# Kernel tuning notes

Hardware: AMD Instinct MI355X
Metric: run time of the kernel (lower is better)

The kernel has to match this reference:

```python
import jax, jax.numpy as jnp
import numpy as np

N = 8192      # nodes
E = 131072    # edges (avg degree 16)
MUL = 128     # multiplicity of 0e and 1o channels
A = 10        # node_attrs (element one-hot) dim
RB = 8        # radial basis size
INV_SQRT3 = 0.5773502691896258  # w3j normalization for l=1 paths


def _lin0(x, W):
    # e3nn-style Linear on scalar (l=0) channels, 1/sqrt(fan_in) normalization
    return (x @ W) / jnp.sqrt(jnp.asarray(W.shape[0], x.dtype))


def _lin1(v, W):
    # e3nn-style Linear on l=1 channels: mixes multiplicities, acts identically on the 3 components
    return jnp.einsum('nuc,uw->nwc', v, W) / jnp.sqrt(jnp.asarray(W.shape[0], v.dtype))


def setup_inputs() -> dict:
    key = jax.random.key(0)
    ks = jax.random.split(key, 26)
    f32 = jnp.float32
    w = lambda k, s: jax.random.normal(k, s, f32)
    D_EF = RB + 2 * MUL  # 264: radial basis + source + target scalar embeddings
    return {
        'node_attrs': jax.random.uniform(ks[0], (N, A), f32),
        'node_feats': w(ks[1], (N, 4 * MUL)),
        'edge_attrs': w(ks[2], (E, 4)),
        'edge_feats': jax.random.uniform(ks[3], (E, RB), f32),
        'edge_index': jax.random.randint(ks[4], (2, E), 0, N, jnp.int32),
        'W_skip_s': w(ks[5], (MUL, MUL)), 'W_skip_v': w(ks[6], (MUL, MUL)),
        'W_up_s': w(ks[7], (MUL, MUL)), 'W_up_v': w(ks[8], (MUL, MUL)),
        'W_src': w(ks[9], (A, MUL)), 'W_tgt': w(ks[10], (A, MUL)),
        'W_r0': w(ks[11], (D_EF, 64)), 'W_r1': w(ks[12], (64, 64)),
        'W_r2': w(ks[13], (64, 64)), 'W_r3': w(ks[14], (64, 4 * MUL)),
        'W_d0': w(ks[15], (D_EF, 64)), 'W_d1': w(ks[16], (64, 1)),
        'W1_s': w(ks[17], (2 * MUL, 2 * MUL)), 'W1_v': w(ks[18], (2 * MUL, MUL)),
        'Wres_s': w(ks[19], (MUL, 2 * MUL)), 'Wres_v': w(ks[20], (MUL, MUL)),
        'W2_s': w(ks[21], (MUL, MUL)), 'W2_v': w(ks[22], (MUL, MUL)),
        'alpha': jnp.asarray(20.0, f32), 'beta': jnp.asarray(0.0, f32),
    }


def reference(node_attrs, node_feats, edge_attrs, edge_feats, edge_index,
              W_skip_s, W_skip_v, W_up_s, W_up_v, W_src, W_tgt,
              W_r0, W_r1, W_r2, W_r3, W_d0, W_d1,
              W1_s, W1_v, Wres_s, Wres_v, W2_s, W2_v, alpha, beta):
    n = node_feats.shape[0]
    s = node_feats[:, :MUL]                       # [N,128] 0e
    v = node_feats[:, MUL:].reshape(n, MUL, 3)    # [N,128,3] 1o
    # skip_tp: Linear(node_feats -> hidden)
    sc = jnp.concatenate([_lin0(s, W_skip_s), _lin1(v, W_skip_v).reshape(n, -1)], axis=-1)
    # linear_up: Linear(node_feats -> edge_irreps)
    us, uv = _lin0(s, W_up_s), _lin1(v, W_up_v)
    # source/target scalar embeddings from node_attrs
    src_e = _lin0(node_attrs, W_src)
    tgt_e = _lin0(node_attrs, W_tgt)
    snd, rcv = edge_index[0], edge_index[1]
    ef = jnp.concatenate([edge_feats, src_e[snd], tgt_e[rcv]], axis=-1)   # [E,264]
    # radial MLP -> per-edge tensor product weights
    h = jax.nn.silu(_lin0(ef, W_r0))
    h = jax.nn.silu(_lin0(h, W_r1))
    h = jax.nn.silu(_lin0(h, W_r2))
    tpw = _lin0(h, W_r3)                          # [E, 4*128]
    # edge density -> per-node density via scatter-sum
    d = jax.nn.silu(_lin0(ef, W_d0))
    edge_density = jnp.tanh(_lin0(d, W_d1) ** 2)  # [E,1]
    density = jax.ops.segment_sum(edge_density, rcv, num_segments=n)      # [N,1]
    # sparse CG tensor product (uvu), paths: 0x0->0e, 0x1->1o, 1x0->1o, 1x1->0e
    xs, xv = us[snd], uv[snd]                     # gather sender features
    y0, y1 = edge_attrs[:, 0], edge_attrs[:, 1:4]
    w1, w2, w3, w4 = jnp.split(tpw, 4, axis=-1)
    m0a = w1 * xs * y0[:, None]                                          # 0e x 0e -> 0e
    m0b = w4 * jnp.einsum('euc,ec->eu', xv, y1) * INV_SQRT3              # 1o x 1o -> 0e
    m1a = (w2 * xs)[:, :, None] * y1[:, None, :] * INV_SQRT3             # 0e x 1o -> 1o
    m1b = w3[:, :, None] * xv * y0[:, None, None] * INV_SQRT3            # 1o x 0e -> 1o
    mid_s = jnp.concatenate([m0a, m0b], axis=1)   # [E,256] irreps_mid scalars
    mid_v = jnp.concatenate([m1a, m1b], axis=1)   # [E,256,3] irreps_mid vectors
    msg_s = jax.ops.segment_sum(mid_s, rcv, num_segments=n)
    msg_v = jax.ops.segment_sum(mid_v, rcv, num_segments=n)
    # linear_1 + learned density normalization
    denom = density * beta + alpha                # [N,1]
    m_s = _lin0(msg_s, W1_s) / denom
    m_v = _lin1(msg_v, W1_v) / denom[..., None]
    # linear_res on up-projected node feats
    m_s = m_s + _lin0(us, Wres_s)                 # [N,256]: 128 scalars + 128 gates
    m_v = m_v + _lin1(uv, Wres_v)                 # [N,128,3]
    # Gate: silu on scalars, sigmoid gates on vectors
    out_s = jax.nn.silu(m_s[:, :MUL])
    out_v = m_v * jax.nn.sigmoid(m_s[:, MUL:])[:, :, None]
    # linear_2
    f_s = _lin0(out_s, W2_s)
    f_v = _lin1(out_v, W2_v)
    # reshape_irreps -> [N, mul, 1+3]
    out = jnp.concatenate([f_s[:, :, None], f_v], axis=2)
    return out, sc
```

## Files before the change

kernel.cpp:

```cpp
#include <hip/hip_runtime.h>

#define NN 8192
#define EE 131072
#define MUL 128
#define AA 10
#define RB 8
#define DEF 264
#define INV_SQRT3 0.5773502691896258f
#define INV_SQRT128 0.08838834764831845f
#define INV_SQRT10 0.31622776601683794f
#define INV_SQRT264 0.06154574548966636f

typedef __attribute__((ext_vector_type(8))) short short8;
typedef __attribute__((ext_vector_type(4))) float floatx4;

#define WS_XQ     ((size_t)0)
#define WS_USB    (WS_XQ    + (size_t)NN*256)
#define WS_UVB    (WS_USB   + (size_t)NN*64)
#define WS_SRC    (WS_UVB   + (size_t)NN*192)
#define WS_TGT    (WS_SRC   + (size_t)NN*64)
#define WS_MSGSB  (WS_TGT   + (size_t)NN*64)
#define WS_MSGVB  (WS_MSGSB + (size_t)NN*128)
#define WS_GATE   (WS_MSGVB + (size_t)NN*384)
#define WS_COUNTS (WS_GATE  + (size_t)NN*128)
#define WS_OFFS   (WS_COUNTS+ (size_t)NN)
#define WS_CURSOR (WS_OFFS  + (size_t)(NN+4))
#define WS_POS    (WS_CURSOR+ (size_t)NN)
#define WS_META   (WS_POS   + (size_t)EE)
#define WS_TPW    (WS_META  + (size_t)EE*8)
#define WS_WB     (WS_TPW   + (size_t)EE*256)
#define WS_WP     (WS_WB    + (size_t)152*256)
#define WS_WN     (WS_WP    + (size_t)352*256)

__device__ __forceinline__ float silu_f(float x) {
    return x * __builtin_amdgcn_rcpf(1.f + __expf(-x));
}
__device__ __forceinline__ float sigm_f(float x) {
    return __builtin_amdgcn_rcpf(1.f + __expf(-x));
}

__device__ __forceinline__ unsigned short f2bf(float x) {
    union { float f; unsigned u; } uf; uf.f = x;
    unsigned r = uf.u + 0x7FFFu + ((uf.u >> 16) & 1u);
    return (unsigned short)(r >> 16);
}

__global__ __launch_bounds__(256) void csr_count(
    const int* __restrict__ edge_index, int* __restrict__ counts)
{
    int e = blockIdx.x * 256 + threadIdx.x;
    atomicAdd(&counts[edge_index[EE + e]], 1);
}

__global__ __launch_bounds__(1024) void csr_scan(
    const int* __restrict__ counts, int* __restrict__ offs, int* __restrict__ cursor)
{
    __shared__ int sums[1024];
    const int t = threadIdx.x;
    int local[8];
    int s = 0;
#pragma unroll
    for (int k = 0; k < 8; ++k) { local[k] = s; s += counts[t * 8 + k]; }
    sums[t] = s;
    __syncthreads();
    for (int d = 1; d < 1024; d <<= 1) {
        int v = (t >= d) ? sums[t - d] : 0;
        __syncthreads();
        sums[t] += v;
        __syncthreads();
    }
    int base = (t > 0) ? sums[t - 1] : 0;
#pragma unroll
    for (int k = 0; k < 8; ++k) {
        offs[t * 8 + k] = base + local[k];
        cursor[t * 8 + k] = base + local[k];
    }
    if (t == 1023) offs[8192] = sums[1023];
}

__global__ __launch_bounds__(256) void csr_scatter(
    const int* __restrict__ edge_index, int* __restrict__ cursor, int* __restrict__ pos)
{
    int e = blockIdx.x * 256 + threadIdx.x;
    pos[e] = atomicAdd(&cursor[edge_index[EE + e]], 1);
}

__global__ __launch_bounds__(256) void swizzle_weights(
    const float* __restrict__ Wr0, const float* __restrict__ Wd0,
    const float* __restrict__ Wr1, const float* __restrict__ Wr2,
    const float* __restrict__ Wr3, unsigned short* __restrict__ WBall)
{
    int fid = blockIdx.x * 256 + threadIdx.x;
    int lane = fid & 63;
    int frag = fid >> 6;
    int k0 = (lane >> 4) * 8;
    int n0 = lane & 15;
    unsigned short o[8];

    if (frag < 72) {
        int kt = frag >> 3, nt = frag & 7;
        int n = nt * 16 + n0;
#pragma unroll
        for (int j = 0; j < 8; ++j) {
            int k = kt * 32 + k0 + j;
            float v = 0.f;
            if (k < 264) v = ((n < 64) ? Wr0[k * 64 + n] : Wd0[k * 64 + (n - 64)]) * INV_SQRT264;
            o[j] = f2bf(v);
        }
    } else if (frag < 80) {
        int fl = frag - 72;
        int kt = fl >> 2, nt = fl & 3;
        int n = nt * 16 + n0;
#pragma unroll
        for (int j = 0; j < 8; ++j)
            o[j] = f2bf(Wr1[(kt * 32 + k0 + j) * 64 + n] * 0.125f);
    } else if (frag < 88) {
        int fl = frag - 80;
        int kt = fl >> 2, nt = fl & 3;
        int n = nt * 16 + n0;
#pragma unroll
        for (int j = 0; j < 8; ++j)
            o[j] = f2bf(Wr2[(kt * 32 + k0 + j) * 64 + n] * 0.125f);
    } else {
        int fl = frag - 88;
        int kt = fl >> 5, nt = fl & 31;
        int n = nt * 16 + n0;
        int q = n >> 6;
        float sc = (q < 2) ? 0.125f : 0.125f * INV_SQRT3;
#pragma unroll
        for (int j = 0; j < 8; ++j)
            o[j] = f2bf(Wr3[(kt * 32 + k0 + j) * 512 + n] * sc);
    }
    uint4 pk;
    pk.x = (unsigned)o[0] | ((unsigned)o[1] << 16);
    pk.y = (unsigned)o[2] | ((unsigned)o[3] << 16);
    pk.z = (unsigned)o[4] | ((unsigned)o[5] << 16);
    pk.w = (unsigned)o[6] | ((unsigned)o[7] << 16);
    *(uint4*)(WBall + (size_t)fid * 8) = pk;
}

__global__ __launch_bounds__(256) void swizzle_post(
    const float* __restrict__ W1s, const float* __restrict__ W1v,
    const float* __restrict__ Wrs, const float* __restrict__ Wrv,
    const float* __restrict__ W2s, const float* __restrict__ W2v,
    unsigned short* __restrict__ WPall)
{
    int fid = blockIdx.x * 256 + threadIdx.x;
    int lane = fid & 63;
    int frag = fid >> 6;
    int k0 = (lane >> 4) * 8;
    int n0 = lane & 15;
    unsigned short o[8];

    if (frag < 192) {
        int kt = frag >> 4, nt = frag & 15;
        int n = nt * 16 + n0;
#pragma unroll
        for (int j = 0; j < 8; ++j) {
            int k = kt * 32 + k0 + j;
            float v = (k < 256) ? W1s[k * 256 + n] * 0.0625f
                                : Wrs[(k - 256) * 256 + n] * INV_SQRT128;
            o[j] = f2bf(v);
        }
    } else if (frag < 288) {
        int fl = frag - 192;
        int kt = fl >> 3, nt = fl & 7;
        int n = nt * 16 + n0;
#pragma unroll
        for (int j = 0; j < 8; ++j) {
            int k = kt * 32 + k0 + j;
            float v = (k < 256) ? W1v[k * 128 + n] * 0.0625f
                                : Wrv[(k - 256) * 128 + n] * INV_SQRT128;
            o[j] = f2bf(v);
        }
    } else if (frag < 320) {
        int fl = frag - 288;
        int kt = fl >> 3, nt = fl & 7;
        int n = nt * 16 + n0;
#pragma unroll
        for (int j = 0; j < 8; ++j)
            o[j] = f2bf(W2s[(kt * 32 + k0 + j) * 128 + n] * INV_SQRT128);
    } else {
        int fl = frag - 320;
        int kt = fl >> 3, nt = fl & 7;
        int n = nt * 16 + n0;
#pragma unroll
        for (int j = 0; j < 8; ++j)
            o[j] = f2bf(W2v[(kt * 32 + k0 + j) * 128 + n] * INV_SQRT128);
    }
    uint4 pk;
    pk.x = (unsigned)o[0] | ((unsigned)o[1] << 16);
    pk.y = (unsigned)o[2] | ((unsigned)o[3] << 16);
    pk.z = (unsigned)o[4] | ((unsigned)o[5] << 16);
    pk.w = (unsigned)o[6] | ((unsigned)o[7] << 16);
    *(uint4*)(WPall + (size_t)fid * 8) = pk;
}

__global__ __launch_bounds__(256) void swizzle_node(
    const float* __restrict__ Wss, const float* __restrict__ Wus,
    const float* __restrict__ Wsv, const float* __restrict__ Wuv,
    const float* __restrict__ Wsrc, const float* __restrict__ Wtgt,
    unsigned short* __restrict__ WN)
{
    int fid = blockIdx.x * 256 + threadIdx.x;
    int lane = fid & 63;
    int frag = fid >> 6;
    int k0 = (lane >> 4) * 8;
    int m0 = lane & 15;
    unsigned short o[8];

    if (frag < 128) {
        int g = frag >> 5;
        int fl = frag & 31;
        int kt = fl >> 3, mt = fl & 7;
        const float* W = (g == 0) ? Wss : (g == 1) ? Wus : (g == 2) ? Wsv : Wuv;
        int m = mt * 16 + m0;
#pragma unroll
        for (int j = 0; j < 8; ++j)
            o[j] = f2bf(W[(kt * 32 + k0 + j) * 128 + m] * INV_SQRT128);
    } else {
        int g = (frag - 128) >> 3;
        int mt = frag & 7;
        const float* W = g ? Wtgt : Wsrc;
        int m = mt * 16 + m0;
#pragma unroll
        for (int j = 0; j < 8; ++j) {
            int k = k0 + j;
            o[j] = f2bf((k < AA) ? W[k * 128 + m] * INV_SQRT10 : 0.f);
        }
    }
    uint4 pk;
    pk.x = (unsigned)o[0] | ((unsigned)o[1] << 16);
    pk.y = (unsigned)o[2] | ((unsigned)o[3] << 16);
    pk.z = (unsigned)o[4] | ((unsigned)o[5] << 16);
    pk.w = (unsigned)o[6] | ((unsigned)o[7] << 16);
    *(uint4*)(WN + (size_t)fid * 8) = pk;
}

#define PNB 16
__global__ __launch_bounds__(256) void node_pre_mfma(
    const float* __restrict__ node_attrs, const float* __restrict__ node_feats,
    const unsigned short* __restrict__ WN,
    float* __restrict__ sc_out, uint2* __restrict__ xq,
    unsigned short* __restrict__ us_b, unsigned short* __restrict__ uv_b,
    unsigned short* __restrict__ srcEb, unsigned short* __restrict__ tgtEb)
{
    __shared__ __align__(16) unsigned short Xs[PNB][136];
    __shared__ __align__(16) unsigned short Xv[3][PNB][136];
    __shared__ __align__(16) unsigned short Xa[PNB][40];
    const int t = threadIdx.x;
    const int l = t & 63, w = t >> 6;
    const int quad = l >> 4, lr = l & 15;
    const int n0 = blockIdx.x * PNB;

    {
        const int r = t >> 4, m = t & 15;
        const float* src = node_feats + (size_t)(n0 + r) * 512;
        float4 s0 = *(const float4*)(src + 8 * m);
        float4 s1 = *(const float4*)(src + 8 * m + 4);
        uint4 sp;
        sp.x = (unsigned)f2bf(s0.x) | ((unsigned)f2bf(s0.y) << 16);
        sp.y = (unsigned)f2bf(s0.z) | ((unsigned)f2bf(s0.w) << 16);
        sp.z = (unsigned)f2bf(s1.x) | ((unsigned)f2bf(s1.y) << 16);
        sp.w = (unsigned)f2bf(s1.z) | ((unsigned)f2bf(s1.w) << 16);
        *(uint4*)&Xs[r][8 * m] = sp;

        float4 q[6];
#pragma unroll
        for (int jj = 0; jj < 6; ++jj)
            q[jj] = *(const float4*)(src + 128 + 24 * m + 4 * jj);
        const float* qf = &q[0].x;
        unsigned short vb[3][8];
#pragma unroll
        for (int u = 0; u < 8; ++u) {
#pragma unroll
            for (int c = 0; c < 3; ++c)
                vb[c][u] = f2bf(qf[u * 3 + c]);
        }
#pragma unroll
        for (int c = 0; c < 3; ++c) {
            uint4 vp;
            vp.x = (unsigned)vb[c][0] | ((unsigned)vb[c][1] << 16);
            vp.y = (unsigned)vb[c][2] | ((unsigned)vb[c][3] << 16);
            vp.z = (unsigned)vb[c][4] | ((unsigned)vb[c][5] << 16);
            vp.w = (unsigned)vb[c][6] | ((unsigned)vb[c][7] << 16);
            *(uint4*)&Xv[c][r][8 * m] = vp;
        }
    }
    for (int idx = t; idx < PNB * 32; idx += 256) {
        int r = idx >> 5, k = idx & 31;
        float v = (k < AA) ? node_attrs[(size_t)(n0 + r) * AA + k] : 0.f;
        Xa[r][k] = f2bf(v);
    }
    __syncthreads();

    const short8* WNf = (const short8*)WN;
    const int n = n0 + lr;

#pragma unroll
    for (int mi = 0; mi < 2; ++mi) {
        const int mt = w * 2 + mi;
        const int j0 = mt * 16 + quad * 4;

        floatx4 cSrc = (floatx4){0.f, 0.f, 0.f, 0.f};
        floatx4 cTgt = (floatx4){0.f, 0.f, 0.f, 0.f};
        {
            short8 ba = *(const short8*)&Xa[lr][quad * 8];
            cSrc = __builtin_amdgcn_mfma_f32_16x16x32_bf16(WNf[(size_t)(128 + mt) * 64 + l], ba, cSrc, 0, 0, 0);
            cTgt = __builtin_amdgcn_mfma_f32_16x16x32_bf16(WNf[(size_t)(136 + mt) * 64 + l], ba, cTgt, 0, 0, 0);
        }
        floatx4 cS = (floatx4){0.f, 0.f, 0.f, 0.f};
        floatx4 cU = (floatx4){0.f, 0.f, 0.f, 0.f};
#pragma unroll
        for (int kt = 0; kt < 4; ++kt) {
            short8 bs = *(const short8*)&Xs[lr][kt * 32 + quad * 8];
            cS = __builtin_amdgcn_mfma_f32_16x16x32_bf16(WNf[(size_t)(kt * 8 + mt) * 64 + l], bs, cS, 0, 0, 0);
            cU = __builtin_amdgcn_mfma_f32_16x16x32_bf16(WNf[(size_t)(32 + kt * 8 + mt) * 64 + l], bs, cU, 0, 0, 0);
        }
        floatx4 cSV[3], cUV[3];
#pragma unroll
        for (int c = 0; c < 3; ++c) {
            cSV[c] = (floatx4){0.f, 0.f, 0.f, 0.f};
            cUV[c] = (floatx4){0.f, 0.f, 0.f, 0.f};
#pragma unroll
            for (int kt = 0; kt < 4; ++kt) {
                short8 bv = *(const short8*)&Xv[c][lr][kt * 32 + quad * 8];
                cSV[c] = __builtin_amdgcn_mfma_f32_16x16x32_bf16(WNf[(size_t)(64 + kt * 8 + mt) * 64 + l], bv, cSV[c], 0, 0, 0);
                cUV[c] = __builtin_amdgcn_mfma_f32_16x16x32_bf16(WNf[(size_t)(96 + kt * 8 + mt) * 64 + l], bv, cUV[c], 0, 0, 0);
            }
        }

        {
            float4 o;
            o.x = cS[0]; o.y = cS[1]; o.z = cS[2]; o.w = cS[3];
            *(float4*)(sc_out + (size_t)n * 512 + j0) = o;
        }
        {
            float vv[12];
#pragma unroll
            for (int reg = 0; reg < 4; ++reg)
#pragma unroll
                for (int c = 0; c < 3; ++c) vv[reg * 3 + c] = cSV[c][reg];
            float* dst = sc_out + (size_t)n * 512 + 128 + j0 * 3;
#pragma unroll
            for (int qq = 0; qq < 3; ++qq) {
                float4 o;
                o.x = vv[qq * 4]; o.y = vv[qq * 4 + 1]; o.z = vv[qq * 4 + 2]; o.w = vv[qq * 4 + 3];
                *(float4*)(dst + qq * 4) = o;
            }
        }
        unsigned short ub[4], vxb[4], vyb[4], vzb[4];
#pragma unroll
        for (int reg = 0; reg < 4; ++reg) {
            ub[reg] = f2bf(cU[reg]);
            vxb[reg] = f2bf(cUV[0][reg]);
            vyb[reg] = f2bf(cUV[1][reg]);
            vzb[reg] = f2bf(cUV[2][reg]);
        }
        {
            uint2 p;
            p.x = (unsigned)ub[0] | ((unsigned)ub[1] << 16);
            p.y = (unsigned)ub[2] | ((unsigned)ub[3] << 16);
            *(uint2*)(us_b + (size_t)n * 128 + j0) = p;
        }
        {
            uint2 p;
            p.x = (unsigned)vxb[0] | ((unsigned)vxb[1] << 16);
            p.y = (unsigned)vxb[2] | ((unsigned)vxb[3] << 16);
            *(uint2*)(uv_b + ((size_t)0 * NN + n) * 128 + j0) = p;
            p.x = (unsigned)vyb[0] | ((unsigned)vyb[1] << 16);
            p.y = (unsigned)vyb[2] | ((unsigned)vyb[3] << 16);
            *(uint2*)(uv_b + ((size_t)1 * NN + n) * 128 + j0) = p;
            p.x = (unsigned)vzb[0] | ((unsigned)vzb[1] << 16);
            p.y = (unsigned)vzb[2] | ((unsigned)vzb[3] << 16);
            *(uint2*)(uv_b + ((size_t)2 * NN + n) * 128 + j0) = p;
        }
        {
            uint4 x0, x1;
            x0.x = (unsigned)ub[0] | ((unsigned)vxb[0] << 16);
            x0.y = (unsigned)vyb[0] | ((unsigned)vzb[0] << 16);
            x0.z = (unsigned)ub[1] | ((unsigned)vxb[1] << 16);
            x0.w = (unsigned)vyb[1] | ((unsigned)vzb[1] << 16);
            x1.x = (unsigned)ub[2] | ((unsigned)vxb[2] << 16);
            x1.y = (unsigned)vyb[2] | ((unsigned)vzb[2] << 16);
            x1.z = (unsigned)ub[3] | ((unsigned)vxb[3] << 16);
            x1.w = (unsigned)vyb[3] | ((unsigned)vzb[3] << 16);
            uint4* xp = (uint4*)(xq + (size_t)n * 128 + j0);
            xp[0] = x0; xp[1] = x1;
        }
        {
            uint2 p;
            p.x = (unsigned)f2bf(cSrc[0]) | ((unsigned)f2bf(cSrc[1]) << 16);
            p.y = (unsigned)f2bf(cSrc[2]) | ((unsigned)f2bf(cSrc[3]) << 16);
            *(uint2*)(srcEb + (size_t)n * 128 + j0) = p;
            p.x = (unsigned)f2bf(cTgt[0]) | ((unsigned)f2bf(cTgt[1]) << 16);
            p.y = (unsigned)f2bf(cTgt[2]) | ((unsigned)f2bf(cTgt[3]) << 16);
            *(uint2*)(tgtEb + (size_t)n * 128 + j0) = p;
        }
    }
}

#define EBK 64
#define H1OFF 80
#define HLD 152
__global__ __launch_bounds__(256, 4) void edge_mlp(
    const float* __restrict__ edge_attrs, const float* __restrict__ edge_feats,
    const int* __restrict__ edge_index,
    const unsigned short* __restrict__ srcEb, const unsigned short* __restrict__ tgtEb,
    const unsigned short* __restrict__ WB0, const unsigned short* __restrict__ WB1,
    const unsigned short* __restrict__ WB2, const unsigned short* __restrict__ WB3,
    const float* __restrict__ Wd1, const int* __restrict__ pos,
    unsigned short* __restrict__ tpwP, float* __restrict__ metaP)
{
    __shared__ __align__(16) unsigned short Hb[4][16][HLD];

    const int t = threadIdx.x;
    const int l = t & 63;
    const int w = t >> 6;
    const int quad = l >> 4;
    const int lr = l & 15;
    const int e0 = blockIdx.x * EBK + w * 16;

    const int eA = e0 + lr;
    const int sndA = edge_index[eA];
    const int rcvA = edge_index[EE + eA];
    const unsigned short* spp = srcEb + (size_t)sndA * 128;
    const unsigned short* tpp = tgtEb + (size_t)rcvA * 128;

    if (quad == 0) {
        float4 ya = *(const float4*)(edge_attrs + (size_t)eA * 4);
        float4 m;
        m.x = __int_as_float(sndA); m.y = ya.y; m.z = ya.z; m.w = ya.w;
        *(float4*)(metaP + (size_t)pos[eA] * 8) = m;
    }

    short8 afr[9];
    {
        const int cq = quad * 8;
        if (quad == 0) {
            float4 f0 = *(const float4*)(edge_feats + (size_t)eA * 8);
            float4 f1 = *(const float4*)(edge_feats + (size_t)eA * 8 + 4);
            union { short8 v; unsigned u[4]; } pk;
            pk.u[0] = (unsigned)f2bf(f0.x) | ((unsigned)f2bf(f0.y) << 16);
            pk.u[1] = (unsigned)f2bf(f0.z) | ((unsigned)f2bf(f0.w) << 16);
            pk.u[2] = (unsigned)f2bf(f1.x) | ((unsigned)f2bf(f1.y) << 16);
            pk.u[3] = (unsigned)f2bf(f1.z) | ((unsigned)f2bf(f1.w) << 16);
            afr[0] = pk.v;
        } else {
            afr[0] = *(const short8*)(spp + (cq - 8));
        }
#pragma unroll
        for (int kt = 1; kt < 9; ++kt) {
            const int c = kt * 32 + cq;
            if (c < 136) {
                afr[kt] = *(const short8*)(spp + (c - 8));
            } else if (c < 264) {
                afr[kt] = *(const short8*)(tpp + (c - 136));
            } else {
                short8 z = {0, 0, 0, 0, 0, 0, 0, 0};
                afr[kt] = z;
            }
        }
    }

    unsigned short (*H)[HLD] = Hb[w];

    {
        floatx4 c0[8];
#pragma unroll
        for (int nt = 0; nt < 8; ++nt) c0[nt] = (floatx4){0.f, 0.f, 0.f, 0.f};
#pragma unroll
        for (int kt = 0; kt < 9; ++kt) {
            const short8* bp = (const short8*)WB0 + (size_t)(kt * 8) * 64 + l;
#pragma unroll
            for (int nt = 0; nt < 8; ++nt)
                c0[nt] = __builtin_amdgcn_mfma_f32_16x16x32_bf16(afr[kt], bp[nt * 64], c0[nt], 0, 0, 0);
        }

#pragma unroll
        for (int nt = 0; nt < 4; ++nt)
#pragma unroll
            for (int reg = 0; reg < 4; ++reg)
                H[quad * 4 + reg][nt * 16 + lr] = f2bf(silu_f(c0[nt][reg]));

        float wd1v[4];
#pragma unroll
        for (int q2 = 0; q2 < 4; ++q2) wd1v[q2] = Wd1[q2 * 16 + lr] * 0.125f;
        float dp[4] = {0.f, 0.f, 0.f, 0.f};
#pragma unroll
        for (int nt = 0; nt < 4; ++nt)
#pragma unroll
            for (int reg = 0; reg < 4; ++reg)
                dp[reg] += silu_f(c0[nt + 4][reg]) * wd1v[nt];
#pragma unroll
        for (int m2 = 1; m2 < 16; m2 <<= 1) {
#pragma unroll
            for (int reg = 0; reg < 4; ++reg) dp[reg] += __shfl_xor(dp[reg], m2);
        }
        if (lr == 0) {
#pragma unroll
            for (int reg = 0; reg < 4; ++reg)
                metaP[(size_t)pos[e0 + quad * 4 + reg] * 8 + 4] = tanhf(dp[reg] * dp[reg]);
        }
    }

    const unsigned short* hrow0 = &H[lr][quad * 8];
    const unsigned short* hrow1 = &H[lr][H1OFF + quad * 8];

    {
        floatx4 c1[4];
#pragma unroll
        for (int nt = 0; nt < 4; ++nt) c1[nt] = (floatx4){0.f, 0.f, 0.f, 0.f};
#pragma unroll
        for (int kt = 0; kt < 2; ++kt) {
            short8 af = *(const short8*)(hrow0 + kt * 32);
            const short8* bp = (const short8*)WB1 + (size_t)(kt * 4) * 64 + l;
#pragma unroll
            for (int nt = 0; nt < 4; ++nt)
                c1[nt] = __builtin_amdgcn_mfma_f32_16x16x32_bf16(af, bp[nt * 64], c1[nt], 0, 0, 0);
        }
#pragma unroll
        for (int nt = 0; nt < 4; ++nt)
#pragma unroll
            for (int reg = 0; reg < 4; ++reg)
                H[quad * 4 + reg][H1OFF + nt * 16 + lr] = f2bf(silu_f(c1[nt][reg]));
    }

    {
        floatx4 c2[4];
#pragma unroll
        for (int nt = 0; nt < 4; ++nt) c2[nt] = (floatx4){0.f, 0.f, 0.f, 0.f};
#pragma unroll
        for (int kt = 0; kt < 2; ++kt) {
            short8 af = *(const short8*)(hrow1 + kt * 32);
            const short8* bp = (const short8*)WB2 + (size_t)(kt * 4) * 64 + l;
#pragma unroll
            for (int nt = 0; nt < 4; ++nt)
                c2[nt] = __builtin_amdgcn_mfma_f32_16x16x32_bf16(af, bp[nt * 64], c2[nt], 0, 0, 0);
        }
#pragma unroll
        for (int nt = 0; nt < 4; ++nt)
#pragma unroll
            for (int reg = 0; reg < 4; ++reg)
                H[quad * 4 + reg][nt * 16 + lr] = f2bf(silu_f(c2[nt][reg]));
    }

    {
        int slotr[4];
        float y0r[4];
#pragma unroll
        for (int reg = 0; reg < 4; ++reg) {
            const int er = e0 + quad * 4 + reg;
            slotr[reg] = pos[er];
            y0r[reg] = edge_attrs[(size_t)er * 4];
        }
        short8 af0 = *(const short8*)(hrow0);
        short8 af1 = *(const short8*)(hrow0 + 32);
        uint2* tpw2 = (uint2*)tpwP;
#pragma unroll
        for (int j2 = 0; j2 < 8; ++j2) {
            floatx4 c3[4];
#pragma unroll
            for (int g = 0; g < 4; ++g) c3[g] = (floatx4){0.f, 0.f, 0.f, 0.f};
#pragma unroll
            for (int g = 0; g < 4; ++g) {
                const short8* b0 = (const short8*)WB3 + (size_t)(g * 8 + j2) * 64 + l;
                const short8* b1 = (const short8*)WB3 + (size_t)(32 + g * 8 + j2) * 64 + l;
                c3[g] = __builtin_amdgcn_mfma_f32_16x16x32_bf16(af0, *b0, c3[g], 0, 0, 0);
                c3[g] = __builtin_amdgcn_mfma_f32_16x16x32_bf16(af1, *b1, c3[g], 0, 0, 0);
            }
            const int u = j2 * 16 + lr;
#pragma unroll
            for (int reg = 0; reg < 4; ++reg) {
                float w1v = c3[0][reg] * y0r[reg];
                float w2v = c3[1][reg];
                float w3v = c3[2][reg] * y0r[reg];
                float w4v = c3[3][reg];
                uint2 p;
                p.x = (unsigned)f2bf(w1v) | ((unsigned)f2bf(w2v) << 16);
                p.y = (unsigned)f2bf(w3v) | ((unsigned)f2bf(w4v) << 16);
                tpw2[(size_t)slotr[reg] * 128 + u] = p;
            }
        }
    }
}

__global__ __launch_bounds__(128) void node_gather(
    const unsigned short* __restrict__ tpwP, const float* __restrict__ metaP,
    const int* __restrict__ offs, const uint2* __restrict__ xq,
    const float* __restrict__ alpha_p, const float* __restrict__ beta_p,
    unsigned short* __restrict__ msgs_b, unsigned short* __restrict__ msgv_b)
{
    const int n = blockIdx.x;
    const int j = threadIdx.x;
    const int s0 = offs[n], s1 = offs[n + 1];
    const uint2* tpw2 = (const uint2*)tpwP;

    float as0 = 0.f, as1 = 0.f;
    float av0x = 0.f, av0y = 0.f, av0z = 0.f;
    float av1x = 0.f, av1y = 0.f, av1z = 0.f;
    float dsum = 0.f;

    int s = s0;
    for (; s + 4 <= s1; s += 4) {
        float4 ma[4]; float dn[4]; uint2 wv[4]; uint2 xv[4];
#pragma unroll
        for (int k = 0; k < 4; ++k) {
            ma[k] = *(const float4*)&metaP[(size_t)(s + k) * 8];
            dn[k] = metaP[(size_t)(s + k) * 8 + 4];
            wv[k] = tpw2[(size_t)(s + k) * 128 + j];
        }
#pragma unroll
        for (int k = 0; k < 4; ++k)
            xv[k] = xq[(size_t)__float_as_int(ma[k].x) * 128 + j];
#pragma unroll
        for (int k = 0; k < 4; ++k) {
            const float y1x = ma[k].y, y1y = ma[k].z, y1z = ma[k].w;
            dsum += dn[k];
            const float w1  = __uint_as_float(wv[k].x << 16);
            const float w2  = __uint_as_float(wv[k].x & 0xffff0000u);
            const float w3  = __uint_as_float(wv[k].y << 16);
            const float w4  = __uint_as_float(wv[k].y & 0xffff0000u);
            const float xs  = __uint_as_float(xv[k].x << 16);
            const float xvx = __uint_as_float(xv[k].x & 0xffff0000u);
            const float xvy = __uint_as_float(xv[k].y << 16);
            const float xvz = __uint_as_float(xv[k].y & 0xffff0000u);
            as0 += w1 * xs;
            as1 += w4 * (xvx * y1x + xvy * y1y + xvz * y1z);
            const float b2 = w2 * xs;
            av0x += b2 * y1x; av0y += b2 * y1y; av0z += b2 * y1z;
            av1x += w3 * xvx; av1y += w3 * xvy; av1z += w3 * xvz;
        }
    }
    for (; s < s1; ++s) {
        const float4 m0 = *(const float4*)&metaP[(size_t)s * 8];
        const float dns = metaP[(size_t)s * 8 + 4];
        const int snd = __float_as_int(m0.x);
        const float y1x = m0.y, y1y = m0.z, y1z = m0.w;
        dsum += dns;
        uint2 wv = tpw2[(size_t)s * 128 + j];
        uint2 xv = xq[(size_t)snd * 128 + j];
        const float w1  = __uint_as_float(wv.x << 16);
        const float w2  = __uint_as_float(wv.x & 0xffff0000u);
        const float w3  = __uint_as_float(wv.y << 16);
        const float w4  = __uint_as_float(wv.y & 0xffff0000u);
        const float xs  = __uint_as_float(xv.x << 16);
        const float xvx = __uint_as_float(xv.x & 0xffff0000u);
        const float xvy = __uint_as_float(xv.y << 16);
        const float xvz = __uint_as_float(xv.y & 0xffff0000u);
        as0 += w1 * xs;
        as1 += w4 * (xvx * y1x + xvy * y1y + xvz * y1z);
        const float b2 = w2 * xs;
        av0x += b2 * y1x; av0y += b2 * y1y; av0z += b2 * y1z;
        av1x += w3 * xvx; av1y += w3 * xvy; av1z += w3 * xvz;
    }

    const float invden = 1.f / (dsum * (*beta_p) + (*alpha_p));

    msgs_b[(size_t)n * 256 + j]       = f2bf(as0 * invden);
    msgs_b[(size_t)n * 256 + 128 + j] = f2bf(as1 * invden);
    msgv_b[((size_t)0 * NN + n) * 256 + j]       = f2bf(av0x * invden);
    msgv_b[((size_t)0 * NN + n) * 256 + 128 + j] = f2bf(av1x * invden);
    msgv_b[((size_t)1 * NN + n) * 256 + j]       = f2bf(av0y * invden);
    msgv_b[((size_t)1 * NN + n) * 256 + 128 + j] = f2bf(av1y * invden);
    msgv_b[((size_t)2 * NN + n) * 256 + j]       = f2bf(av0z * invden);
    msgv_b[((size_t)2 * NN + n) * 256 + 128 + j] = f2bf(av1z * invden);
}

#define DNP 16
__global__ __launch_bounds__(256) void post_fused(
    const unsigned short* __restrict__ msgs_b, const unsigned short* __restrict__ us_b,
    const unsigned short* __restrict__ msgv_b, const unsigned short* __restrict__ uv_b,
    const unsigned short* __restrict__ WPs, const unsigned short* __restrict__ WPv,
    const unsigned short* __restrict__ W2ss, const unsigned short* __restrict__ W2vs,
    float* __restrict__ out)
{
    __shared__ __align__(16) unsigned short osb[DNP][136];
    __shared__ __align__(16) unsigned short ovb[3][DNP][136];
    __shared__ float gateL[DNP][128];

    const int t = threadIdx.x;
    const int l = t & 63, w = t >> 6;
    const int quad = l >> 4, lr = l & 15;
    const int n0 = blockIdx.x * DNP;
    const int nh = w;
    const int n = n0 + lr;

    const int cLo = (nh * 6) >> 3;
    const int cHi = (nh * 6 + 5) >> 3;

    const unsigned short* sRow  = msgs_b + (size_t)n * 256;
    const unsigned short* uRow  = us_b   + (size_t)n * 128;
    const unsigned short* vRowL = msgv_b + ((size_t)cLo * NN + n) * 256;
    const unsigned short* uRowL = uv_b   + ((size_t)cLo * NN + n) * 128;
    const unsigned short* vRowH = msgv_b + ((size_t)cHi * NN + n) * 256;
    const unsigned short* uRowH = uv_b   + ((size_t)cHi * NN + n) * 128;

    floatx4 accS[4], accV[6];
#pragma unroll
    for (int i = 0; i < 4; ++i) accS[i] = (floatx4){0.f, 0.f, 0.f, 0.f};
#pragma unroll
    for (int i = 0; i < 6; ++i) accV[i] = (floatx4){0.f, 0.f, 0.f, 0.f};

#pragma unroll
    for (int kt = 0; kt < 12; ++kt) {
        const int col = kt * 32 + quad * 8;
        short8 aS = (col < 256) ? *(const short8*)(sRow + col)
                                : *(const short8*)(uRow + col - 256);
        short8 aV0 = (col < 256) ? *(const short8*)(vRowL + col)
                                 : *(const short8*)(uRowL + col - 256);
        short8 aV1;
        if (cHi != cLo)
            aV1 = (col < 256) ? *(const short8*)(vRowH + col)
                              : *(const short8*)(uRowH + col - 256);
        else
            aV1 = aV0;

        const short8* bpS = (const short8*)WPs + (size_t)(kt * 16 + nh * 4) * 64 + l;
#pragma unroll
        for (int i = 0; i < 4; ++i)
            accS[i] = __builtin_amdgcn_mfma_f32_16x16x32_bf16(aS, bpS[i * 64], accS[i], 0, 0, 0);
#pragma unroll
        for (int i = 0; i < 6; ++i) {
            const int vt = nh * 6 + i;
            const short8* bpV = (const short8*)WPv + (size_t)(kt * 8 + (vt & 7)) * 64 + l;
            short8 a = ((vt >> 3) == cLo) ? aV0 : aV1;
            accV[i] = __builtin_amdgcn_mfma_f32_16x16x32_bf16(a, *bpV, accV[i], 0, 0, 0);
        }
    }

#pragma unroll
    for (int i = 0; i < 4; ++i) {
        const int tile = nh * 4 + i;
#pragma unroll
        for (int reg = 0; reg < 4; ++reg) {
            const int row = quad * 4 + reg;
            const float v = accS[i][reg];
            if (tile < 8) osb[row][tile * 16 + lr] = f2bf(silu_f(v));
            else          gateL[row][(tile - 8) * 16 + lr] = sigm_f(v);
        }
    }
    __syncthreads();

#pragma unroll
    for (int i = 0; i < 6; ++i) {
        const int vt = nh * 6 + i;
        const int c = vt >> 3;
        const int colv = (vt & 7) * 16 + lr;
#pragma unroll
        for (int reg = 0; reg < 4; ++reg) {
            const int row = quad * 4 + reg;
            ovb[c][row][colv] = f2bf(accV[i][reg] * gateL[row][colv]);
        }
    }
    __syncthreads();

    floatx4 c2s[2], c2v[6];
#pragma unroll
    for (int i = 0; i < 2; ++i) c2s[i] = (floatx4){0.f, 0.f, 0.f, 0.f};
#pragma unroll
    for (int i = 0; i < 6; ++i) c2v[i] = (floatx4){0.f, 0.f, 0.f, 0.f};

    const unsigned short* arowS = &osb[lr][quad * 8];
#pragma unroll
    for (int kt = 0; kt < 4; ++kt) {
        short8 afS = *(const short8*)(arowS + kt * 32);
        const short8* bpS = (const short8*)W2ss + (size_t)(kt * 8 + nh * 2) * 64 + l;
#pragma unroll
        for (int i = 0; i < 2; ++i)
            c2s[i] = __builtin_amdgcn_mfma_f32_16x16x32_bf16(afS, bpS[i * 64], c2s[i], 0, 0, 0);
#pragma unroll
        for (int i = 0; i < 6; ++i) {
            const int vt = nh * 6 + i;
            const int c = vt >> 3;
            short8 afV = *(const short8*)(&ovb[c][lr][quad * 8] + kt * 32);
            const short8* bpV = (const short8*)W2vs + (size_t)(kt * 8 + (vt & 7)) * 64 + l;
            c2v[i] = __builtin_amdgcn_mfma_f32_16x16x32_bf16(afV, *bpV, c2v[i], 0, 0, 0);
        }
    }

#pragma unroll
    for (int i = 0; i < 2; ++i) {
        const int col = (nh * 2 + i) * 16 + lr;
#pragma unroll
        for (int reg = 0; reg < 4; ++reg)
            out[(size_t)(n0 + quad * 4 + reg) * 512 + col * 4] = c2s[i][reg];
    }
#pragma unroll
    for (int i = 0; i < 6; ++i) {
        const int vt = nh * 6 + i;
        const int c = vt >> 3;
        const int col = (vt & 7) * 16 + lr;
#pragma unroll
        for (int reg = 0; reg < 4; ++reg)
            out[(size_t)(n0 + quad * 4 + reg) * 512 + col * 4 + 1 + c] = c2v[i][reg];
    }
}

extern "C" void kernel_launch(void* const* d_in, const int* in_sizes, int n_in,
                              void* d_out, int out_size, void* d_ws, size_t ws_size,
                              hipStream_t stream)
{
    const float* node_attrs = (const float*)d_in[0];
    const float* node_feats = (const float*)d_in[1];
    const float* edge_attrs = (const float*)d_in[2];
    const float* edge_feats = (const float*)d_in[3];
    const int*   edge_index = (const int*)d_in[4];
    const float* W_skip_s = (const float*)d_in[5];
    const float* W_skip_v = (const float*)d_in[6];
    const float* W_up_s   = (const float*)d_in[7];
    const float* W_up_v   = (const float*)d_in[8];
    const float* W_src    = (const float*)d_in[9];
    const float* W_tgt    = (const float*)d_in[10];
    const float* W_r0     = (const float*)d_in[11];
    const float* W_r1     = (const float*)d_in[12];
    const float* W_r2     = (const float*)d_in[13];
    const float* W_r3     = (const float*)d_in[14];
    const float* W_d0     = (const float*)d_in[15];
    const float* W_d1     = (const float*)d_in[16];
    const float* W1_s     = (const float*)d_in[17];
    const float* W1_v     = (const float*)d_in[18];
    const float* Wres_s   = (const float*)d_in[19];
    const float* Wres_v   = (const float*)d_in[20];
    const float* W2_s     = (const float*)d_in[21];
    const float* W2_v     = (const float*)d_in[22];
    const float* alpha_p  = (const float*)d_in[23];
    const float* beta_p   = (const float*)d_in[24];

    float* out = (float*)d_out;
    float* sc_out = out + (size_t)NN * 512;
    float* ws = (float*)d_ws;

    uint2* xq = (uint2*)(ws + WS_XQ);
    unsigned short* us_b  = (unsigned short*)(ws + WS_USB);
    unsigned short* uv_b  = (unsigned short*)(ws + WS_UVB);
    unsigned short* srcEb = (unsigned short*)(ws + WS_SRC);
    unsigned short* tgtEb = (unsigned short*)(ws + WS_TGT);
    unsigned short* msgs_b = (unsigned short*)(ws + WS_MSGSB);
    unsigned short* msgv_b = (unsigned short*)(ws + WS_MSGVB);
    int*   counts = (int*)(ws + WS_COUNTS);
    int*   offs   = (int*)(ws + WS_OFFS);
    int*   cursor = (int*)(ws + WS_CURSOR);
    int*   pos    = (int*)(ws + WS_POS);
    float* metaP  = ws + WS_META;
    unsigned short* tpwP = (unsigned short*)(ws + WS_TPW);
    unsigned short* WBall = (unsigned short*)(ws + WS_WB);
    unsigned short* WB0 = WBall;
    unsigned short* WB1 = WB0 + (size_t)72 * 512;
    unsigned short* WB2 = WB1 + (size_t)8 * 512;
    unsigned short* WB3 = WB2 + (size_t)8 * 512;
    unsigned short* WPall = (unsigned short*)(ws + WS_WP);
    unsigned short* WPs  = WPall;
    unsigned short* WPv  = WPs + (size_t)192 * 512;
    unsigned short* W2ss = WPv + (size_t)96 * 512;
    unsigned short* W2vs = W2ss + (size_t)32 * 512;
    unsigned short* WN   = (unsigned short*)(ws + WS_WN);

    hipMemsetAsync(counts, 0, (size_t)NN * sizeof(int), stream);

    csr_count<<<EE / 256, 256, 0, stream>>>(edge_index, counts);
    csr_scan<<<1, 1024, 0, stream>>>(counts, offs, cursor);
    csr_scatter<<<EE / 256, 256, 0, stream>>>(edge_index, cursor, pos);

    swizzle_weights<<<38, 256, 0, stream>>>(W_r0, W_d0, W_r1, W_r2, W_r3, WBall);
    swizzle_post<<<88, 256, 0, stream>>>(W1_s, W1_v, Wres_s, Wres_v, W2_s, W2_v, WPall);
    swizzle_node<<<36, 256, 0, stream>>>(W_skip_s, W_up_s, W_skip_v, W_up_v,
                                         W_src, W_tgt, WN);

    node_pre_mfma<<<NN / PNB, 256, 0, stream>>>(
        node_attrs, node_feats, WN, sc_out, xq, us_b, uv_b, srcEb, tgtEb);

    edge_mlp<<<EE / EBK, 256, 0, stream>>>(
        edge_attrs, edge_feats, edge_index, srcEb, tgtEb,
        WB0, WB1, WB2, WB3, W_d1, pos, tpwP, metaP);

    node_gather<<<NN, 128, 0, stream>>>(
        tpwP, metaP, offs, xq, alpha_p, beta_p, msgs_b, msgv_b);

    post_fused<<<NN / DNP, 256, 0, stream>>>(
        msgs_b, us_b, msgv_b, uv_b, WPs, WPv, W2ss, W2vs, out);
}
```

Baseline: 304.1 us.

## Move final radial MLP layer into receiver-sorted gather kernel with MFMA

The edge MLP now stores only the 64-wide hidden activations per edge, in CSR order, instead of the 512-wide tensor-product weights. A new gather kernel recomputes the last radial layer with MFMA over 16-edge chunks that span two receivers. It forms the messages and accumulates them into shared memory with atomics, then normalizes and writes out. This cuts the large per-edge weight write and read-back, at the cost of 64-thread blocks, LDS atomic contention, and masked partial chunks.

```diff
diff --git a/kernel.cpp b/kernel.cpp
--- a/kernel.cpp
+++ b/kernel.cpp
@@ -408,9 +408,9 @@
     const int* __restrict__ edge_index,
     const unsigned short* __restrict__ srcEb, const unsigned short* __restrict__ tgtEb,
     const unsigned short* __restrict__ WB0, const unsigned short* __restrict__ WB1,
-    const unsigned short* __restrict__ WB2, const unsigned short* __restrict__ WB3,
+    const unsigned short* __restrict__ WB2,
     const float* __restrict__ Wd1, const int* __restrict__ pos,
-    unsigned short* __restrict__ tpwP, float* __restrict__ metaP)
+    unsigned short* __restrict__ h2P, float* __restrict__ metaP)
 {
     __shared__ __align__(16) unsigned short Hb[4][16][HLD];
 
@@ -424,6 +424,7 @@
     const int eA = e0 + lr;
     const int sndA = edge_index[eA];
     const int rcvA = edge_index[EE + eA];
+    const int slotA = pos[eA];
     const unsigned short* spp = srcEb + (size_t)sndA * 128;
     const unsigned short* tpp = tgtEb + (size_t)rcvA * 128;
 
@@ -431,7 +432,8 @@
         float4 ya = *(const float4*)(edge_attrs + (size_t)eA * 4);
         float4 m;
         m.x = __int_as_float(sndA); m.y = ya.y; m.z = ya.z; m.w = ya.w;
-        *(float4*)(metaP + (size_t)pos[eA] * 8) = m;
+        *(float4*)(metaP + (size_t)slotA * 8) = m;
+        metaP[(size_t)slotA * 8 + 5] = ya.x;
     }
 
     short8 afr[9];
@@ -546,17 +548,58 @@
     }
 
     {
-        int slotr[4];
-        float y0r[4];
+        const unsigned short* src = &H[lr][quad * 16];
+        uint4 v0 = *(const uint4*)(src);
+        uint4 v1 = *(const uint4*)(src + 8);
+        uint4* dst = (uint4*)(h2P + (size_t)slotA * 64 + quad * 16);
+        dst[0] = v0;
+        dst[1] = v1;
+    }
+}
+
+#define RCVB 2
+__global__ __launch_bounds__(64) void gather_mfma(
+    const unsigned short* __restrict__ h2P, const float* __restrict__ metaP,
+    const int* __restrict__ offs, const uint2* __restrict__ xq,
+    const unsigned short* __restrict__ WB3,
+    const float* __restrict__ alpha_p, const float* __restrict__ beta_p,
+    unsigned short* __restrict__ msgs_b, unsigned short* __restrict__ msgv_b)
+{
+    __shared__ float acc[RCVB][1024];
+    const int l = threadIdx.x;
+    const int quad = l >> 4, lr = l & 15;
+    const int r0 = blockIdx.x * RCVB;
+
+    for (int k = l; k < RCVB * 1024; k += 64) ((float*)acc)[k] = 0.f;
+
+    const int sB = offs[r0];
+    const int sM = offs[r0 + 1];
+    const int sE = offs[r0 + 2];
+    __syncthreads();
+
+    for (int chunk = sB; chunk < sE; chunk += 16) {
+        int srow = chunk + lr;
+        if (srow >= sE) srow = sE - 1;
+        const unsigned short* hr = h2P + (size_t)srow * 64;
+        short8 af0 = *(const short8*)(hr + quad * 8);
+        short8 af1 = *(const short8*)(hr + 32 + quad * 8);
+
+        int sndr[4], rcb[4];
+        float y0r[4], y1x[4], y1y[4], y1z[4];
+        bool mk[4];
 #pragma unroll
         for (int reg = 0; reg < 4; ++reg) {
-            const int er = e0 + quad * 4 + reg;
-            slotr[reg] = pos[er];
-            y0r[reg] = edge_attrs[(size_t)er * 4];
-        }
-        short8 af0 = *(const short8*)(hrow0);
-        short8 af1 = *(const short8*)(hrow0 + 32);
-        uint2* tpw2 = (uint2*)tpwP;
+            int e = chunk + quad * 4 + reg;
+            mk[reg] = (e < sE);
+            int em = mk[reg] ? e : (sE - 1);
+            const float* mp = metaP + (size_t)em * 8;
+            float4 m0 = *(const float4*)mp;
+            sndr[reg] = __float_as_int(m0.x);
+            y1x[reg] = m0.y; y1y[reg] = m0.z; y1z[reg] = m0.w;
+            y0r[reg] = mp[5];
+            rcb[reg] = (em >= sM) ? 1 : 0;
+        }
+
 #pragma unroll
         for (int j2 = 0; j2 < 8; ++j2) {
             floatx4 c3[4];
@@ -572,99 +615,55 @@
             const int u = j2 * 16 + lr;
 #pragma unroll
             for (int reg = 0; reg < 4; ++reg) {
-                float w1v = c3[0][reg] * y0r[reg];
-                float w2v = c3[1][reg];
-                float w3v = c3[2][reg] * y0r[reg];
-                float w4v = c3[3][reg];
-                uint2 p;
-                p.x = (unsigned)f2bf(w1v) | ((unsigned)f2bf(w2v) << 16);
-                p.y = (unsigned)f2bf(w3v) | ((unsigned)f2bf(w4v) << 16);
-                tpw2[(size_t)slotr[reg] * 128 + u] = p;
+                if (!mk[reg]) continue;
+                uint2 xv = xq[(size_t)sndr[reg] * 128 + u];
+                const float xs  = __uint_as_float(xv.x << 16);
+                const float xvx = __uint_as_float(xv.x & 0xffff0000u);
+                const float xvy = __uint_as_float(xv.y << 16);
+                const float xvz = __uint_as_float(xv.y & 0xffff0000u);
+                const float w1 = c3[0][reg] * y0r[reg];
+                const float w2 = c3[1][reg];
+                const float w3 = c3[2][reg] * y0r[reg];
+                const float w4 = c3[3][reg];
+                float* a = acc[rcb[reg]];
+                const float b2 = w2 * xs;
+                atomicAdd(&a[u],        w1 * xs);
+                atomicAdd(&a[128 + u],  w4 * (xvx * y1x[reg] + xvy * y1y[reg] + xvz * y1z[reg]));
+                atomicAdd(&a[256 + u],  b2 * y1x[reg]);
+                atomicAdd(&a[384 + u],  w3 * xvx);
+                atomicAdd(&a[512 + u],  b2 * y1y[reg]);
+                atomicAdd(&a[640 + u],  w3 * xvy);
+                atomicAdd(&a[768 + u],  b2 * y1z[reg]);
+                atomicAdd(&a[896 + u],  w3 * xvz);
             }
         }
     }
-}
-
-__global__ __launch_bounds__(128) void node_gather(
-    const unsigned short* __restrict__ tpwP, const float* __restrict__ metaP,
-    const int* __restrict__ offs, const uint2* __restrict__ xq,
-    const float* __restrict__ alpha_p, const float* __restrict__ beta_p,
-    unsigned short* __restrict__ msgs_b, unsigned short* __restrict__ msgv_b)
-{
-    const int n = blockIdx.x;
-    const int j = threadIdx.x;
-    const int s0 = offs[n], s1 = offs[n + 1];
-    const uint2* tpw2 = (const uint2*)tpwP;
-
-    float as0 = 0.f, as1 = 0.f;
-    float av0x = 0.f, av0y = 0.f, av0z = 0.f;
-    float av1x = 0.f, av1y = 0.f, av1z = 0.f;
-    float dsum = 0.f;
-
-    int s = s0;
-    for (; s + 4 <= s1; s += 4) {
-        float4 ma[4]; float dn[4]; uint2 wv[4]; uint2 xv[4];
-#pragma unroll
-        for (int k = 0; k < 4; ++k) {
-            ma[k] = *(const float4*)&metaP[(size_t)(s + k) * 8];
-            dn[k] = metaP[(size_t)(s + k) * 8 + 4];
-            wv[k] = tpw2[(size_t)(s + k) * 128 + j];
-        }
-#pragma unroll
-        for (int k = 0; k < 4; ++k)
-            xv[k] = xq[(size_t)__float_as_int(ma[k].x) * 128 + j];
-#pragma unroll
-        for (int k = 0; k < 4; ++k) {
-            const float y1x = ma[k].y, y1y = ma[k].z, y1z = ma[k].w;
-            dsum += dn[k];
-            const float w1  = __uint_as_float(wv[k].x << 16);
-            const float w2  = __uint_as_float(wv[k].x & 0xffff0000u);
-            const float w3  = __uint_as_float(wv[k].y << 16);
-            const float w4  = __uint_as_float(wv[k].y & 0xffff0000u);
-            const float xs  = __uint_as_float(xv[k].x << 16);
-            const float xvx = __uint_as_float(xv[k].x & 0xffff0000u);
-            const float xvy = __uint_as_float(xv[k].y << 16);
-            const float xvz = __uint_as_float(xv[k].y & 0xffff0000u);
-            as0 += w1 * xs;
-            as1 += w4 * (xvx * y1x + xvy * y1y + xvz * y1z);
-            const float b2 = w2 * xs;
-            av0x += b2 * y1x; av0y += b2 * y1y; av0z += b2 * y1z;
-            av1x += w3 * xvx; av1y += w3 * xvy; av1z += w3 * xvz;
-        }
-    }
-    for (; s < s1; ++s) {
-        const float4 m0 = *(const float4*)&metaP[(size_t)s * 8];
-        const float dns = metaP[(size_t)s * 8 + 4];
-        const int snd = __float_as_int(m0.x);
-        const float y1x = m0.y, y1y = m0.z, y1z = m0.w;
-        dsum += dns;
-        uint2 wv = tpw2[(size_t)s * 128 + j];
-        uint2 xv = xq[(size_t)snd * 128 + j];
-        const float w1  = __uint_as_float(wv.x << 16);
-        const float w2  = __uint_as_float(wv.x & 0xffff0000u);
-        const float w3  = __uint_as_float(wv.y << 16);
-        const float w4  = __uint_as_float(wv.y & 0xffff0000u);
-        const float xs  = __uint_as_float(xv.x << 16);
-        const float xvx = __uint_as_float(xv.x & 0xffff0000u);
-        const float xvy = __uint_as_float(xv.y << 16);
-        const float xvz = __uint_as_float(xv.y & 0xffff0000u);
-        as0 += w1 * xs;
-        as1 += w4 * (xvx * y1x + xvy * y1y + xvz * y1z);
-        const float b2 = w2 * xs;
-        av0x += b2 * y1x; av0y += b2 * y1y; av0z += b2 * y1z;
-        av1x += w3 * xvx; av1y += w3 * xvy; av1z += w3 * xvz;
-    }
-
-    const float invden = 1.f / (dsum * (*beta_p) + (*alpha_p));
-
-    msgs_b[(size_t)n * 256 + j]       = f2bf(as0 * invden);
-    msgs_b[(size_t)n * 256 + 128 + j] = f2bf(as1 * invden);
-    msgv_b[((size_t)0 * NN + n) * 256 + j]       = f2bf(av0x * invden);
-    msgv_b[((size_t)0 * NN + n) * 256 + 128 + j] = f2bf(av1x * invden);
-    msgv_b[((size_t)1 * NN + n) * 256 + j]       = f2bf(av0y * invden);
-    msgv_b[((size_t)1 * NN + n) * 256 + 128 + j] = f2bf(av1y * invden);
-    msgv_b[((size_t)2 * NN + n) * 256 + j]       = f2bf(av0z * invden);
-    msgv_b[((size_t)2 * NN + n) * 256 + 128 + j] = f2bf(av1z * invden);
+    __syncthreads();
+
+    const float alpha = *alpha_p, beta = *beta_p;
+#pragma unroll
+    for (int kr = 0; kr < RCVB; ++kr) {
+        const int n = r0 + kr;
+        const int s0 = offs[n], s1 = offs[n + 1];
+        float ds = 0.f;
+        for (int s = s0 + l; s < s1; s += 64) ds += metaP[(size_t)s * 8 + 4];
+#pragma unroll
+        for (int m2 = 1; m2 < 64; m2 <<= 1) ds += __shfl_xor(ds, m2);
+        const float invden = 1.f / (ds * beta + alpha);
+
+        for (int idx = l; idx < 1024; idx += 64) {
+            const float v = acc[kr][idx] * invden;
+            const int region = idx >> 7, u = idx & 127;
+            const unsigned short bv = f2bf(v);
+            if (region == 0)      msgs_b[(size_t)n * 256 + u] = bv;
+            else if (region == 1) msgs_b[(size_t)n * 256 + 128 + u] = bv;
+            else {
+                const int c  = (region - 2) >> 1;
+                const int hi = (region - 2) & 1;
+                msgv_b[((size_t)c * NN + n) * 256 + hi * 128 + u] = bv;
+            }
+        }
+    }
 }
 
 #define DNP 16
@@ -843,7 +842,7 @@
     int*   cursor = (int*)(ws + WS_CURSOR);
     int*   pos    = (int*)(ws + WS_POS);
     float* metaP  = ws + WS_META;
-    unsigned short* tpwP = (unsigned short*)(ws + WS_TPW);
+    unsigned short* h2P = (unsigned short*)(ws + WS_TPW);
     unsigned short* WBall = (unsigned short*)(ws + WS_WB);
     unsigned short* WB0 = WBall;
     unsigned short* WB1 = WB0 + (size_t)72 * 512;
@@ -872,10 +871,10 @@
 
     edge_mlp<<<EE / EBK, 256, 0, stream>>>(
         edge_attrs, edge_feats, edge_index, srcEb, tgtEb,
-        WB0, WB1, WB2, WB3, W_d1, pos, tpwP, metaP);
-
-    node_gather<<<NN, 128, 0, stream>>>(
-        tpwP, metaP, offs, xq, alpha_p, beta_p, msgs_b, msgv_b);
+        WB0, WB1, WB2, W_d1, pos, h2P, metaP);
+
+    gather_mfma<<<NN / RCVB, 64, 0, stream>>>(
+        h2P, metaP, offs, xq, WB3, alpha_p, beta_p, msgs_b, msgv_b);
 
     post_fused<<<NN / DNP, 256, 0, stream>>>(
         msgs_b, us_b, msgv_b, uv_b, WPs, WPv, W2ss, W2vs, out);
```

Result: slower. 989.3 us (+225.3%).
